# Kernel optimization log

Measured on AMD Instinct MI355X. Metric: run time of the kernel, lower is better.

Reference implementation:

```python
import jax, jax.numpy as jnp
import numpy as np
import math

B, S = 1, 2048
HID = 4096
NH = 32            # total query heads
NKV = 8            # total kv heads
D = HID // NH      # 128 head_dim
WIN = 1024         # sliding window (layer_idx=1 is odd and < num_layers//2)
LAYER = 1
THETA = 10000.0
LAMBDA_INIT = 0.8 - 0.6 * math.exp(-0.3 * LAYER)
SCALE = D ** -0.5
EPS = 1e-5
OP = NH * D + 2 * NKV * D  # Wqkv output size


def setup_inputs() -> dict:
    key = jax.random.key(0)
    ks = jax.random.split(key, 9)
    std = 0.02
    return {
        "hidden_states": jax.random.normal(ks[0], (B * S, HID), jnp.float32),
        "positions": jnp.tile(jnp.arange(S, dtype=jnp.int32), B),
        "Wqkv_w": jax.random.normal(ks[1], (OP, HID), jnp.float32) * std,
        "Wqkv_b": jnp.zeros((OP,), jnp.float32),
        "out_w": jax.random.normal(ks[2], (HID, NH * D), jnp.float32) * std,
        "out_b": jnp.zeros((HID,), jnp.float32),
        "lambda_q1": jax.random.normal(ks[3], (D,), jnp.float32) * 0.1,
        "lambda_k1": jax.random.normal(ks[4], (D,), jnp.float32) * 0.1,
        "lambda_q2": jax.random.normal(ks[5], (D,), jnp.float32) * 0.1,
        "lambda_k2": jax.random.normal(ks[6], (D,), jnp.float32) * 0.1,
        "subln_w": jnp.ones((2 * D,), jnp.float32),
    }


def _rope(x, pos):
    # neox-style rotary; x: [N, H, D], pos: [N]
    half = D // 2
    inv_freq = 1.0 / (THETA ** (jnp.arange(half, dtype=jnp.float32) / half))
    ang = pos.astype(jnp.float32)[:, None] * inv_freq[None, :]      # [N, half]
    cos = jnp.cos(ang)[:, None, :]
    sin = jnp.sin(ang)[:, None, :]
    x1, x2 = x[..., :half], x[..., half:]
    return jnp.concatenate([x1 * cos - x2 * sin, x2 * cos + x1 * sin], axis=-1)


def _probs(q, k, mask):
    # q: [B,S,Hq,D], k: [B,S,Hkv,D] -> softmax probs [B,Hq,S,S] with GQA repeat
    g = q.shape[2] // k.shape[2]
    k = jnp.repeat(k, g, axis=2)
    scores = jnp.einsum('bqhd,bkhd->bhqk', q, k) * SCALE
    scores = jnp.where(mask, scores, -1e30)
    return jax.nn.softmax(scores, axis=-1)


def _pv(p, v, g):
    # p: [B,Hq,S,S], v: [B,S,Hkv,D]
    v = jnp.repeat(v, g, axis=2)
    return jnp.einsum('bhqk,bkhd->bqhd', p, v)


def reference(hidden_states, positions, Wqkv_w, Wqkv_b, out_w, out_b,
              lambda_q1, lambda_k1, lambda_q2, lambda_k2, subln_w):
    qkv = hidden_states @ Wqkv_w.T + Wqkv_b                 # [N, OP]
    q, k, v = jnp.split(qkv, [NH * D, NH * D + NKV * D], axis=-1)
    q = q.reshape(-1, NH, D)
    k = k.reshape(-1, NKV, D)
    v = v.reshape(-1, NKV, D)
    q = _rope(q, positions)
    k = _rope(k, positions)

    q = q.reshape(B, S, NH, D)
    k = k.reshape(B, S, NKV, D)
    v = v.reshape(B, S, NKV, D)
    # split_heads: '(H two) D' -> even heads = group1, odd heads = group2
    q1, q2 = q[:, :, 0::2], q[:, :, 1::2]
    k1, k2 = k[:, :, 0::2], k[:, :, 1::2]
    v1, v2 = v[:, :, 0::2], v[:, :, 1::2]

    i = jnp.arange(S)[:, None]
    j = jnp.arange(S)[None, :]
    mask = (j <= i) & ((i - j) < WIN)                        # causal + sliding window

    g = (NH // 2) // (NKV // 2)
    p1 = _probs(q1, k1, mask)
    p2 = _probs(q2, k2, mask)
    a11 = _pv(p1, v1, g)
    a12 = _pv(p1, v2, g)
    a21 = _pv(p2, v1, g)
    a22 = _pv(p2, v2, g)

    attn1 = jnp.concatenate([a11, a12], axis=-1)             # [B,S,NH/2,2D]
    attn2 = jnp.concatenate([a21, a22], axis=-1)

    lam = (jnp.exp(jnp.sum(lambda_q1 * lambda_k1))
           - jnp.exp(jnp.sum(lambda_q2 * lambda_k2)) + LAMBDA_INIT)
    attn = attn1 - lam * attn2

    # subln: RMSNorm over last dim (2*head_dim)
    var = jnp.mean(attn * attn, axis=-1, keepdims=True)
    attn = attn * jax.lax.rsqrt(var + EPS) * subln_w
    attn = attn * (1.0 - LAMBDA_INIT)

    attn = attn.reshape(B * S, NH * D)
    return attn @ out_w.T + out_b
```

## Files before the change

### kernel.cpp

```cpp
#include <hip/hip_runtime.h>

typedef unsigned short u16;
typedef __attribute__((ext_vector_type(8))) short bf16x8;
typedef __attribute__((ext_vector_type(4))) float f32x4;
typedef __attribute__((ext_vector_type(4))) unsigned short us4;
typedef __attribute__((ext_vector_type(8))) unsigned short us8;

#define S_LEN 2048
#define QKV_P 6144
#define WIN_SZ 1024
#define SCALE_F 0.08838834764831845f
#define LAMBDA_INIT_F 0.35550906759096925f
#define ONE_MINUS_LI_F 0.6444909324090308f

__device__ __forceinline__ u16 f2bf(float f) {
    union { float f; unsigned int u; } v; v.f = f;
    unsigned int u = v.u;
    return (u16)((u + 0x7fffu + ((u >> 16) & 1u)) >> 16);
}
__device__ __forceinline__ float bf2f(u16 u) {
    union { unsigned int u; float f; } v; v.u = ((unsigned int)u) << 16; return v.f;
}
__device__ __forceinline__ void gload16(const void* g, void* l) {
    __builtin_amdgcn_global_load_lds(
        (const __attribute__((address_space(1))) unsigned int*)g,
        (__attribute__((address_space(3))) unsigned int*)l, 16, 0, 0);
}

__global__ __launch_bounds__(256)
void conv_f32_bf16(const float* __restrict__ src, u16* __restrict__ dst, int n4) {
    for (int i = blockIdx.x * 256 + threadIdx.x; i < n4; i += gridDim.x * 256) {
        float4 v = ((const float4*)src)[i];
        us4 h;
        h.x = f2bf(v.x); h.y = f2bf(v.y); h.z = f2bf(v.z); h.w = f2bf(v.w);
        ((us4*)dst)[i] = h;
    }
}

template<int NR>
__device__ __forceinline__ void stage_half(const u16* __restrict__ src, int K,
                                           int gRowBase, int kcol0,
                                           u16* slot, int tid, int wid) {
#pragma unroll
    for (int g = 0; g < 2; ++g) {
        if (g * 128 + wid * 16 < NR) {
            int row = g * 128 + (tid >> 2);
            int cc = (tid & 3) ^ ((row >> 1) & 3);
            gload16(src + (size_t)(gRowBase + row) * K + kcol0 + cc * 8,
                    slot + g * 4096 + wid * 512);
        }
    }
}

__device__ __forceinline__ bf16x8 ldfrag(const u16* slot, int row, int l4) {
    int pc = l4 ^ ((row >> 1) & 3);
    return *(const bf16x8*)(slot + row * 32 + pc * 8);
}

template<int NF>
__device__ __forceinline__ void gemm_wait(int wid) {
    if constexpr (NF == 3) {
        if (wid < 4) asm volatile("s_waitcnt vmcnt(4)" ::: "memory");
        else         asm volatile("s_waitcnt vmcnt(3)" ::: "memory");
    } else if constexpr (NF == 2) {
        asm volatile("s_waitcnt vmcnt(3)" ::: "memory");
    } else {
        asm volatile("s_waitcnt vmcnt(4)" ::: "memory");
    }
}

template<int NF, int OUT_BF16>
__global__ __launch_bounds__(512)
__attribute__((amdgpu_waves_per_eu(2, 2)))
void gemm8p(const u16* __restrict__ A, const u16* __restrict__ W,
            const float* __restrict__ bias, void* __restrict__ Cv,
            int M, int N, int K, int nbx) {
    constexpr int BN = NF * 64;
    constexpr int BSLOT = NF * 2048;
    __shared__ u16 lds[32768 + 4 * BSLOT];

    const int tid = threadIdx.x;
    const int wid = tid >> 6, lane = tid & 63;
    const int wr = wid >> 2, wc = wid & 3;
    const int l15 = lane & 15, l4 = lane >> 4;

    const int nwg = gridDim.x;
    const int q8 = nwg >> 3;
    const int swz = (blockIdx.x & 7) * q8 + (blockIdx.x >> 3);
    const int bx = swz % nbx, by = swz / nbx;
    const int rowBase = by * 256;
    const int colBase = bx * BN;

    const int NT = K >> 6;

    u16* const baseA = lds;
    u16* const baseB = lds + 32768;

    f32x4 acc[8][NF] = {};

    stage_half<256>(A, K, rowBase, 0,  baseA + 0 * 8192, tid, wid);
    stage_half<BN> (W, K, colBase, 0,  baseB + 0 * BSLOT, tid, wid);
    stage_half<256>(A, K, rowBase, 32, baseA + 1 * 8192, tid, wid);
    stage_half<BN> (W, K, colBase, 32, baseB + 1 * BSLOT, tid, wid);
    stage_half<256>(A, K, rowBase, 64, baseA + 2 * 8192, tid, wid);
    stage_half<BN> (W, K, colBase, 64, baseB + 2 * BSLOT, tid, wid);
    gemm_wait<NF>(wid);
    __builtin_amdgcn_s_barrier();

    for (int t = 0; t < NT; ++t) {
        const int b = t & 1;
        const int bn = b ^ 1;
        u16* const A0 = baseA + (b * 2 + 0) * 8192;
        u16* const A1 = baseA + (b * 2 + 1) * 8192;
        u16* const B0 = baseB + (b * 2 + 0) * BSLOT;
        u16* const B1 = baseB + (b * 2 + 1) * BSLOT;

        bf16x8 af[4], bfv[NF];

#pragma unroll
        for (int m = 0; m < 4; ++m) af[m] = ldfrag(A0, wr * 128 + m * 16 + l15, l4);
#pragma unroll
        for (int n = 0; n < NF; ++n) bfv[n] = ldfrag(B0, wc * (NF * 16) + n * 16 + l15, l4);
        if (t + 1 < NT)
            stage_half<256>(A, K, rowBase, (t + 1) * 64 + 32, baseA + (bn * 2 + 1) * 8192, tid, wid);
        __builtin_amdgcn_s_barrier();
        __builtin_amdgcn_s_setprio(1);
#pragma unroll
        for (int m = 0; m < 4; ++m)
#pragma unroll
            for (int n = 0; n < NF; ++n)
                acc[m][n] = __builtin_amdgcn_mfma_f32_16x16x32_bf16(af[m], bfv[n], acc[m][n], 0, 0, 0);
        __builtin_amdgcn_s_setprio(0);
        __builtin_amdgcn_s_barrier();

#pragma unroll
        for (int m = 0; m < 4; ++m) af[m] = ldfrag(A0, wr * 128 + (m + 4) * 16 + l15, l4);
        if (t + 1 < NT)
            stage_half<BN>(W, K, colBase, (t + 1) * 64 + 32, baseB + (bn * 2 + 1) * BSLOT, tid, wid);
        __builtin_amdgcn_s_barrier();
        __builtin_amdgcn_s_setprio(1);
#pragma unroll
        for (int m = 0; m < 4; ++m)
#pragma unroll
            for (int n = 0; n < NF; ++n)
                acc[m + 4][n] = __builtin_amdgcn_mfma_f32_16x16x32_bf16(af[m], bfv[n], acc[m + 4][n], 0, 0, 0);
        __builtin_amdgcn_s_setprio(0);
        __builtin_amdgcn_s_barrier();

#pragma unroll
        for (int m = 0; m < 4; ++m) af[m] = ldfrag(A1, wr * 128 + m * 16 + l15, l4);
#pragma unroll
        for (int n = 0; n < NF; ++n) bfv[n] = ldfrag(B1, wc * (NF * 16) + n * 16 + l15, l4);
        if (t + 2 < NT)
            stage_half<256>(A, K, rowBase, (t + 2) * 64, baseA + (b * 2 + 0) * 8192, tid, wid);
        __builtin_amdgcn_s_barrier();
        __builtin_amdgcn_s_setprio(1);
#pragma unroll
        for (int m = 0; m < 4; ++m)
#pragma unroll
            for (int n = 0; n < NF; ++n)
                acc[m][n] = __builtin_amdgcn_mfma_f32_16x16x32_bf16(af[m], bfv[n], acc[m][n], 0, 0, 0);
        __builtin_amdgcn_s_setprio(0);
        __builtin_amdgcn_s_barrier();

#pragma unroll
        for (int m = 0; m < 4; ++m) af[m] = ldfrag(A1, wr * 128 + (m + 4) * 16 + l15, l4);
        if (t + 2 < NT)
            stage_half<BN>(W, K, colBase, (t + 2) * 64, baseB + (b * 2 + 0) * BSLOT, tid, wid);
        __builtin_amdgcn_s_barrier();
        __builtin_amdgcn_s_setprio(1);
#pragma unroll
        for (int m = 0; m < 4; ++m)
#pragma unroll
            for (int n = 0; n < NF; ++n)
                acc[m + 4][n] = __builtin_amdgcn_mfma_f32_16x16x32_bf16(af[m], bfv[n], acc[m + 4][n], 0, 0, 0);
        __builtin_amdgcn_s_setprio(0);
        if (t + 2 < NT) gemm_wait<NF>(wid);
        else            asm volatile("s_waitcnt vmcnt(0)" ::: "memory");
        __builtin_amdgcn_s_barrier();
    }

#pragma unroll
    for (int n = 0; n < NF; ++n) {
        int col = colBase + wc * (NF * 16) + n * 16 + l15;
        float bs = bias[col];
#pragma unroll
        for (int m = 0; m < 8; ++m)
#pragma unroll
            for (int rr = 0; rr < 4; ++rr) {
                int rowi = rowBase + wr * 128 + m * 16 + l4 * 4 + rr;
                float v = acc[m][n][rr] + bs;
                if (OUT_BF16) ((u16*)Cv)[(size_t)rowi * N + col] = f2bf(v);
                else          ((float*)Cv)[(size_t)rowi * N + col] = v;
            }
    }
}

__global__ __launch_bounds__(256)
void rope_bf16(u16* __restrict__ qkv, const int* __restrict__ positions) {
    const int row = blockIdx.x;
    const float pos = (float)positions[row];
    for (int idx = threadIdx.x; idx < 640; idx += 256) {
        int head = idx >> 4;
        int g = idx & 15;
        int base = (head < 32) ? head * 128 : 4096 + (head - 32) * 128;
        u16* p = qkv + (size_t)row * QKV_P + base + g * 4;
        us4 x1 = *(us4*)p;
        us4 x2 = *(us4*)(p + 64);
#pragma unroll
        for (int j = 0; j < 4; ++j) {
            float inv_freq = __expf(-(float)(g * 4 + j) * (9.210340371976184f / 64.0f));
            float ang = pos * inv_freq;
            float s, c;
            sincosf(ang, &s, &c);
            float a = bf2f(x1[j]), b = bf2f(x2[j]);
            x1[j] = f2bf(a * c - b * s);
            x2[j] = f2bf(b * c + a * s);
        }
        *(us4*)p = x1;
        *(us4*)(p + 64) = x2;
    }
}

__global__ __launch_bounds__(256)
void vtrans(const u16* __restrict__ qkv, u16* __restrict__ vt) {
    __shared__ u16 T[128 * 72];
    const int s0 = blockIdx.x * 64;
    const int a = blockIdx.y;
    const u16* src = qkv + 5120 + a * 128;
#pragma unroll
    for (int it = 0; it < 4; ++it) {
        int idx = it * 256 + threadIdx.x;
        int s = idx >> 4;
        int c8 = idx & 15;
        us8 v = *(const us8*)(src + (size_t)(s0 + s) * QKV_P + c8 * 8);
        int sc = s >> 3, su = s & 7;
#pragma unroll
        for (int j = 0; j < 8; ++j) {
            int d = c8 * 8 + j;
            T[d * 72 + ((sc ^ ((d >> 3) & 7)) * 8 + su)] = v[j];
        }
    }
    __syncthreads();
#pragma unroll
    for (int it = 0; it < 4; ++it) {
        int idx = it * 256 + threadIdx.x;
        int d = idx >> 3, sc = idx & 7;
        us8 v = *(const us8*)&T[d * 72 + ((sc ^ ((d >> 3) & 7)) * 8)];
        *(us8*)(vt + (size_t)a * 262144 + (size_t)d * 2048 + s0 + sc * 8) = v;
    }
}

__global__ __launch_bounds__(512)
__attribute__((amdgpu_waves_per_eu(2, 2)))
void attn_bf16(const u16* __restrict__ qkv, const u16* __restrict__ vtg,
               u16* __restrict__ attnb,
               const float* __restrict__ lq1, const float* __restrict__ lk1,
               const float* __restrict__ lq2, const float* __restrict__ lk2,
               const float* __restrict__ subln) {
    __shared__ u16 Kb[2][2][64 * 128];
    __shared__ u16 Vb[2][2][128 * 64];
    __shared__ u16 Pw[8][16 * 64];

    const int tid = threadIdx.x;
    const int w = tid >> 6, lane = tid & 63;
    const int l15 = lane & 15, l4 = lane >> 4;

    const int qb = blockIdx.x & 15;
    const int h  = blockIdx.x >> 4;
    const int q0 = qb * 128;
    const int h1 = 2 * h, h2 = 2 * h + 1;
    const int a1 = 2 * (h >> 2), a2 = a1 + 1;

    bf16x8 q1f[4], q2f[4];
    {
        int qrow = q0 + w * 16 + l15;
        const u16* qp1 = qkv + (size_t)qrow * QKV_P + h1 * 128;
        const u16* qp2 = qkv + (size_t)qrow * QKV_P + h2 * 128;
#pragma unroll
        for (int kk = 0; kk < 4; ++kk) {
            q1f[kk] = *(const bf16x8*)(qp1 + kk * 32 + l4 * 8);
            q2f[kk] = *(const bf16x8*)(qp2 + kk * 32 + l4 * 8);
        }
    }

    f32x4 a11[8] = {}, a12[8] = {}, a21[8] = {}, a22[8] = {};
    float m1[4], l1[4], m2[4], l2[4];
#pragma unroll
    for (int r = 0; r < 4; ++r) { m1[r] = -1e30f; l1[r] = 0.f; m2[r] = -1e30f; l2[r] = 0.f; }

    const int kr4 = lane >> 4;
    const int kc  = lane & 15;
    const int vd8 = lane >> 3;
    const int vc  = lane & 7;

    const int tbeg = (qb >= 8) ? ((q0 - (WIN_SZ - 1)) >> 6) : 0;
    const int tend = (q0 + 127) >> 6;

#define STAGE_TILE(T, NB)                                                      \
    {                                                                          \
        const int kv0s = (T) * 64;                                             \
        _Pragma("unroll")                                                      \
        for (int s = 0; s < 2; ++s) {                                          \
            int ch = w * 2 + s;                                                \
            int krow = ch * 4 + kr4;                                           \
            int kcs = (kc ^ (krow & 7)) * 8;                                   \
            const u16* kbase = qkv + (size_t)(kv0s + krow) * QKV_P + 4096;     \
            gload16(kbase + a1 * 128 + kcs, &Kb[NB][0][ch * 512]);             \
            gload16(kbase + a2 * 128 + kcs, &Kb[NB][1][ch * 512]);             \
            int vdrow = ch * 8 + vd8;                                          \
            int vcs = (vc ^ (vdrow & 7)) * 8;                                  \
            const u16* vbase = vtg + (size_t)vdrow * 2048 + kv0s + vcs;        \
            gload16(vbase + (size_t)a1 * 262144, &Vb[NB][0][ch * 512]);        \
            gload16(vbase + (size_t)a2 * 262144, &Vb[NB][1][ch * 512]);        \
        }                                                                      \
    }

    STAGE_TILE(tbeg, 0);
    asm volatile("s_waitcnt vmcnt(0)" ::: "memory");
    __builtin_amdgcn_s_barrier();
    asm volatile("" ::: "memory");

    int cb = 0;
    for (int t = tbeg; t <= tend; ++t) {
        const int kv0 = t * 64;

        if (t < tend) STAGE_TILE(t + 1, cb ^ 1);

        f32x4 sc1[4], sc2[4];
        __builtin_amdgcn_s_setprio(1);
#pragma unroll
        for (int c = 0; c < 4; ++c) {
            f32x4 s1 = {0.f, 0.f, 0.f, 0.f};
            f32x4 s2 = {0.f, 0.f, 0.f, 0.f};
#pragma unroll
            for (int kk = 0; kk < 4; ++kk) {
                int off = (c * 16 + l15) * 128 + (((kk * 4 + l4) ^ (l15 & 7)) * 8);
                bf16x8 kf1 = *(const bf16x8*)&Kb[cb][0][off];
                bf16x8 kf2 = *(const bf16x8*)&Kb[cb][1][off];
                s1 = __builtin_amdgcn_mfma_f32_16x16x32_bf16(q1f[kk], kf1, s1, 0, 0, 0);
                s2 = __builtin_amdgcn_mfma_f32_16x16x32_bf16(q2f[kk], kf2, s2, 0, 0, 0);
            }
            sc1[c] = s1; sc2[c] = s2;
        }
        __builtin_amdgcn_s_setprio(0);

        const bool dz = (t >= tend - 1);
        const bool wz = (qb >= 8) && (t <= tbeg + 1);
        if (dz) {
#pragma unroll
            for (int c = 0; c < 4; ++c) {
                int j = kv0 + c * 16 + l15;
#pragma unroll
                for (int r = 0; r < 4; ++r) {
                    int i = q0 + w * 16 + l4 * 4 + r;
                    if (j > i) { sc1[c][r] = -1e30f; sc2[c][r] = -1e30f; }
                }
            }
        } else if (wz) {
#pragma unroll
            for (int c = 0; c < 4; ++c) {
                int j = kv0 + c * 16 + l15;
#pragma unroll
                for (int r = 0; r < 4; ++r) {
                    int i = q0 + w * 16 + l4 * 4 + r;
                    if (i - j >= WIN_SZ) { sc1[c][r] = -1e30f; sc2[c][r] = -1e30f; }
                }
            }
        }

        float rmax1[4], rmax2[4];
#pragma unroll
        for (int r = 0; r < 4; ++r) {
            rmax1[r] = fmaxf(fmaxf(sc1[0][r], sc1[1][r]), fmaxf(sc1[2][r], sc1[3][r]));
            rmax2[r] = fmaxf(fmaxf(sc2[0][r], sc2[1][r]), fmaxf(sc2[2][r], sc2[3][r]));
        }
#pragma unroll
        for (int msk = 1; msk < 16; msk <<= 1)
#pragma unroll
            for (int r = 0; r < 4; ++r) {
                rmax1[r] = fmaxf(rmax1[r], __shfl_xor(rmax1[r], msk));
                rmax2[r] = fmaxf(rmax2[r], __shfl_xor(rmax2[r], msk));
            }
        bool need = false;
#pragma unroll
        for (int r = 0; r < 4; ++r)
            need = need || (rmax1[r] > m1[r] + 32.0f) || (rmax2[r] > m2[r] + 32.0f);
        if (__any(need)) {
            float f1[4], f2[4];
#pragma unroll
            for (int r = 0; r < 4; ++r) {
                float nm1 = fmaxf(m1[r], rmax1[r]);
                float nm2 = fmaxf(m2[r], rmax2[r]);
                f1[r] = __expf((m1[r] - nm1) * SCALE_F);
                f2[r] = __expf((m2[r] - nm2) * SCALE_F);
                m1[r] = nm1; m2[r] = nm2;
                l1[r] *= f1[r]; l2[r] *= f2[r];
            }
#pragma unroll
            for (int f = 0; f < 8; ++f)
#pragma unroll
                for (int r = 0; r < 4; ++r) {
                    a11[f][r] *= f1[r]; a12[f][r] *= f1[r];
                    a21[f][r] *= f2[r]; a22[f][r] *= f2[r];
                }
        }

        float rs1[4] = {0.f, 0.f, 0.f, 0.f}, rs2[4] = {0.f, 0.f, 0.f, 0.f};
#pragma unroll
        for (int c = 0; c < 4; ++c) {
            int col = c * 16 + l15;
#pragma unroll
            for (int r = 0; r < 4; ++r) {
                int prow = l4 * 4 + r;
                float p1 = __expf((sc1[c][r] - m1[r]) * SCALE_F);
                float p2 = __expf((sc2[c][r] - m2[r]) * SCALE_F);
                if (wz) {
                    if (m1[r] < -1e29f) p1 = 0.f;
                    if (m2[r] < -1e29f) p2 = 0.f;
                }
                rs1[r] += p1; rs2[r] += p2;
                sc2[c][r] = p2;
                int pco = ((col >> 3) ^ (prow & 7)) * 8 + (col & 7);
                Pw[w][prow * 64 + pco] = f2bf(p1);
            }
        }
#pragma unroll
        for (int msk = 1; msk < 16; msk <<= 1)
#pragma unroll
            for (int r = 0; r < 4; ++r) {
                rs1[r] += __shfl_xor(rs1[r], msk);
                rs2[r] += __shfl_xor(rs2[r], msk);
            }
#pragma unroll
        for (int r = 0; r < 4; ++r) { l1[r] += rs1[r]; l2[r] += rs2[r]; }

        __builtin_amdgcn_s_setprio(1);
#pragma unroll
        for (int kk = 0; kk < 2; ++kk) {
            int pch = ((kk * 4 + l4) ^ (l15 & 7)) * 8;
            bf16x8 pa = *(const bf16x8*)&Pw[w][l15 * 64 + pch];
#pragma unroll
            for (int f = 0; f < 8; ++f) {
                int off = (f * 16 + l15) * 64 + (((kk * 4 + l4) ^ (l15 & 7)) * 8);
                bf16x8 vb1 = *(const bf16x8*)&Vb[cb][0][off];
                bf16x8 vb2 = *(const bf16x8*)&Vb[cb][1][off];
                a11[f] = __builtin_amdgcn_mfma_f32_16x16x32_bf16(pa, vb1, a11[f], 0, 0, 0);
                a12[f] = __builtin_amdgcn_mfma_f32_16x16x32_bf16(pa, vb2, a12[f], 0, 0, 0);
            }
        }
        __builtin_amdgcn_s_setprio(0);

#pragma unroll
        for (int c = 0; c < 4; ++c) {
            int col = c * 16 + l15;
#pragma unroll
            for (int r = 0; r < 4; ++r) {
                int prow = l4 * 4 + r;
                int pco = ((col >> 3) ^ (prow & 7)) * 8 + (col & 7);
                Pw[w][prow * 64 + pco] = f2bf(sc2[c][r]);
            }
        }
        __builtin_amdgcn_s_setprio(1);
#pragma unroll
        for (int kk = 0; kk < 2; ++kk) {
            int pch = ((kk * 4 + l4) ^ (l15 & 7)) * 8;
            bf16x8 pa = *(const bf16x8*)&Pw[w][l15 * 64 + pch];
#pragma unroll
            for (int f = 0; f < 8; ++f) {
                int off = (f * 16 + l15) * 64 + (((kk * 4 + l4) ^ (l15 & 7)) * 8);
                bf16x8 vb1 = *(const bf16x8*)&Vb[cb][0][off];
                bf16x8 vb2 = *(const bf16x8*)&Vb[cb][1][off];
                a21[f] = __builtin_amdgcn_mfma_f32_16x16x32_bf16(pa, vb1, a21[f], 0, 0, 0);
                a22[f] = __builtin_amdgcn_mfma_f32_16x16x32_bf16(pa, vb2, a22[f], 0, 0, 0);
            }
        }
        __builtin_amdgcn_s_setprio(0);

        asm volatile("s_waitcnt vmcnt(0)" ::: "memory");
        __builtin_amdgcn_s_barrier();
        asm volatile("" ::: "memory");
        cb ^= 1;
    }

    float s1v = lq1[lane] * lk1[lane] + lq1[lane + 64] * lk1[lane + 64];
    float s2v = lq2[lane] * lk2[lane] + lq2[lane + 64] * lk2[lane + 64];
#pragma unroll
    for (int msk = 1; msk < 64; msk <<= 1) {
        s1v += __shfl_xor(s1v, msk);
        s2v += __shfl_xor(s2v, msk);
    }
    const float lam = __expf(s1v) - __expf(s2v) + LAMBDA_INIT_F;

    float sw0[8], sw1[8];
#pragma unroll
    for (int f = 0; f < 8; ++f) {
        sw0[f] = subln[f * 16 + l15];
        sw1[f] = subln[128 + f * 16 + l15];
    }

#pragma unroll
    for (int r = 0; r < 4; ++r) {
        float inv1 = 1.0f / l1[r];
        float inv2 = 1.0f / l2[r];
        float o0[8], o1[8];
        float ssq = 0.f;
#pragma unroll
        for (int f = 0; f < 8; ++f) {
            o0[f] = a11[f][r] * inv1 - lam * (a21[f][r] * inv2);
            o1[f] = a12[f][r] * inv1 - lam * (a22[f][r] * inv2);
            ssq += o0[f] * o0[f] + o1[f] * o1[f];
        }
#pragma unroll
        for (int msk = 1; msk < 16; msk <<= 1) ssq += __shfl_xor(ssq, msk);
        float scale = rsqrtf(ssq * (1.0f / 256.0f) + 1e-5f) * ONE_MINUS_LI_F;
        int row = q0 + w * 16 + l4 * 4 + r;
        u16* op = attnb + (size_t)row * 4096 + h * 256;
#pragma unroll
        for (int f = 0; f < 8; ++f) {
            op[f * 16 + l15]       = f2bf(o0[f] * scale * sw0[f]);
            op[128 + f * 16 + l15] = f2bf(o1[f] * scale * sw1[f]);
        }
    }
}

extern "C" void kernel_launch(void* const* d_in, const int* in_sizes, int n_in,
                              void* d_out, int out_size, void* d_ws, size_t ws_size,
                              hipStream_t stream) {
    const float* hidden    = (const float*)d_in[0];
    const int*   positions = (const int*)d_in[1];
    const float* Wqkv_w    = (const float*)d_in[2];
    const float* Wqkv_b    = (const float*)d_in[3];
    const float* out_w     = (const float*)d_in[4];
    const float* out_b     = (const float*)d_in[5];
    const float* lq1       = (const float*)d_in[6];
    const float* lk1       = (const float*)d_in[7];
    const float* lq2       = (const float*)d_in[8];
    const float* lk2       = (const float*)d_in[9];
    const float* subln     = (const float*)d_in[10];
    float* out = (float*)d_out;

    u16* ws0   = (u16*)d_ws;
    u16* hb    = ws0;
    u16* wqb   = ws0 + 8388608;
    u16* qkvb  = ws0 + 33554432;
    u16* attnb = ws0;
    u16* owb   = ws0 + 8388608;
    u16* vt    = ws0 + 25165824;

    conv_f32_bf16<<<2048, 256, 0, stream>>>(hidden, hb, 2048 * 4096 / 4);
    conv_f32_bf16<<<2048, 256, 0, stream>>>(Wqkv_w, wqb, 6144 * 4096 / 4);

    gemm8p<3, 1><<<256, 512, 0, stream>>>(hb, wqb, Wqkv_b, qkvb, 2048, 6144, 4096, 32);

    rope_bf16<<<S_LEN, 256, 0, stream>>>(qkvb, positions);
    vtrans<<<dim3(32, 8), 256, 0, stream>>>(qkvb, vt);

    conv_f32_bf16<<<2048, 256, 0, stream>>>(out_w, owb, 4096 * 4096 / 4);

    attn_bf16<<<256, 512, 0, stream>>>(qkvb, vt, attnb, lq1, lk1, lq2, lk2, subln);

    gemm8p<2, 0><<<256, 512, 0, stream>>>(attnb, owb, out_b, out, 2048, 4096, 4096, 32);
}
```

Before: 407.6 us.

## Split attention heads across wave groups and halve query tile per block

The attention kernel now uses 64-row query tiles and 512 blocks. Within a block, waves 0-3 handle the first differential head and waves 4-7 the second, where before every wave handled both heads. Each wave keeps one softmax state and two PV accumulators, which lowers register pressure, and the two halves are combined through shared memory at the end. Heavy blocks are issued first to balance the load. In exchange, each K/V tile is loaded by more blocks, and the final combine adds a shared-memory pass and a block-wide barrier.

```diff
diff --git a/kernel.cpp b/kernel.cpp
--- a/kernel.cpp
+++ b/kernel.cpp
@@ -258,61 +258,61 @@
                const float* __restrict__ lq1, const float* __restrict__ lk1,
                const float* __restrict__ lq2, const float* __restrict__ lk2,
                const float* __restrict__ subln) {
-    __shared__ u16 Kb[2][2][64 * 128];
-    __shared__ u16 Vb[2][2][128 * 64];
-    __shared__ u16 Pw[8][16 * 64];
+    __shared__ u16 smem[73728];
+#define KBUF(b, st) (smem + ((b) * 2 + (st)) * 8192)
+#define VBUF(b, st) (smem + 32768 + ((b) * 2 + (st)) * 8192)
 
     const int tid = threadIdx.x;
     const int w = tid >> 6, lane = tid & 63;
+    const int g = w & 3, sid = w >> 2;
     const int l15 = lane & 15, l4 = lane >> 4;
-
-    const int qb = blockIdx.x & 15;
-    const int h  = blockIdx.x >> 4;
-    const int q0 = qb * 128;
-    const int h1 = 2 * h, h2 = 2 * h + 1;
+    u16* const Pw = smem + 65536 + w * 1024;
+
+    int qb, h;
+    {
+        int i = blockIdx.x;
+        if (i < 256) { qb = 16 + (i & 15); h = i >> 4; }
+        else         { int j = i - 256; qb = j & 15; h = j >> 4; }
+    }
+    const int q0 = qb * 64;
     const int a1 = 2 * (h >> 2), a2 = a1 + 1;
 
-    bf16x8 q1f[4], q2f[4];
+    bf16x8 qf[4];
     {
-        int qrow = q0 + w * 16 + l15;
-        const u16* qp1 = qkv + (size_t)qrow * QKV_P + h1 * 128;
-        const u16* qp2 = qkv + (size_t)qrow * QKV_P + h2 * 128;
-#pragma unroll
-        for (int kk = 0; kk < 4; ++kk) {
-            q1f[kk] = *(const bf16x8*)(qp1 + kk * 32 + l4 * 8);
-            q2f[kk] = *(const bf16x8*)(qp2 + kk * 32 + l4 * 8);
-        }
-    }
-
-    f32x4 a11[8] = {}, a12[8] = {}, a21[8] = {}, a22[8] = {};
-    float m1[4], l1[4], m2[4], l2[4];
-#pragma unroll
-    for (int r = 0; r < 4; ++r) { m1[r] = -1e30f; l1[r] = 0.f; m2[r] = -1e30f; l2[r] = 0.f; }
-
-    const int kr4 = lane >> 4;
-    const int kc  = lane & 15;
-    const int vd8 = lane >> 3;
-    const int vc  = lane & 7;
-
-    const int tbeg = (qb >= 8) ? ((q0 - (WIN_SZ - 1)) >> 6) : 0;
-    const int tend = (q0 + 127) >> 6;
+        int qrow = q0 + g * 16 + l15;
+        const u16* qp = qkv + (size_t)qrow * QKV_P + (2 * h + sid) * 128;
+#pragma unroll
+        for (int kk = 0; kk < 4; ++kk)
+            qf[kk] = *(const bf16x8*)(qp + kk * 32 + l4 * 8);
+    }
+
+    f32x4 aV1[8] = {}, aV2[8] = {};
+    float m[4], l[4];
+#pragma unroll
+    for (int r = 0; r < 4; ++r) { m[r] = -1e30f; l[r] = 0.f; }
+
+    const int kr4 = lane >> 4, kc = lane & 15;
+    const int vd8 = lane >> 3, vc = lane & 7;
+
+    const int tbeg = (qb >= 16) ? (qb - 16) : 0;
+    const int tend = qb;
 
 #define STAGE_TILE(T, NB)                                                      \
     {                                                                          \
         const int kv0s = (T) * 64;                                             \
         _Pragma("unroll")                                                      \
-        for (int s = 0; s < 2; ++s) {                                          \
-            int ch = w * 2 + s;                                                \
+        for (int s2 = 0; s2 < 2; ++s2) {                                       \
+            int ch = w * 2 + s2;                                               \
             int krow = ch * 4 + kr4;                                           \
             int kcs = (kc ^ (krow & 7)) * 8;                                   \
             const u16* kbase = qkv + (size_t)(kv0s + krow) * QKV_P + 4096;     \
-            gload16(kbase + a1 * 128 + kcs, &Kb[NB][0][ch * 512]);             \
-            gload16(kbase + a2 * 128 + kcs, &Kb[NB][1][ch * 512]);             \
+            gload16(kbase + a1 * 128 + kcs, KBUF(NB, 0) + ch * 512);           \
+            gload16(kbase + a2 * 128 + kcs, KBUF(NB, 1) + ch * 512);           \
             int vdrow = ch * 8 + vd8;                                          \
             int vcs = (vc ^ (vdrow & 7)) * 8;                                  \
             const u16* vbase = vtg + (size_t)vdrow * 2048 + kv0s + vcs;        \
-            gload16(vbase + (size_t)a1 * 262144, &Vb[NB][0][ch * 512]);        \
-            gload16(vbase + (size_t)a2 * 262144, &Vb[NB][1][ch * 512]);        \
+            gload16(vbase + (size_t)a1 * 262144, VBUF(NB, 0) + ch * 512);      \
+            gload16(vbase + (size_t)a2 * 262144, VBUF(NB, 1) + ch * 512);      \
         }                                                                      \
     }
 
@@ -327,34 +327,31 @@
 
         if (t < tend) STAGE_TILE(t + 1, cb ^ 1);
 
-        f32x4 sc1[4], sc2[4];
+        f32x4 sc[4];
+        const u16* Kc = KBUF(cb, sid);
         __builtin_amdgcn_s_setprio(1);
 #pragma unroll
         for (int c = 0; c < 4; ++c) {
             f32x4 s1 = {0.f, 0.f, 0.f, 0.f};
-            f32x4 s2 = {0.f, 0.f, 0.f, 0.f};
 #pragma unroll
             for (int kk = 0; kk < 4; ++kk) {
                 int off = (c * 16 + l15) * 128 + (((kk * 4 + l4) ^ (l15 & 7)) * 8);
-                bf16x8 kf1 = *(const bf16x8*)&Kb[cb][0][off];
-                bf16x8 kf2 = *(const bf16x8*)&Kb[cb][1][off];
-                s1 = __builtin_amdgcn_mfma_f32_16x16x32_bf16(q1f[kk], kf1, s1, 0, 0, 0);
-                s2 = __builtin_amdgcn_mfma_f32_16x16x32_bf16(q2f[kk], kf2, s2, 0, 0, 0);
-            }
-            sc1[c] = s1; sc2[c] = s2;
+                s1 = __builtin_amdgcn_mfma_f32_16x16x32_bf16(qf[kk], *(const bf16x8*)&Kc[off], s1, 0, 0, 0);
+            }
+            sc[c] = s1;
         }
         __builtin_amdgcn_s_setprio(0);
 
-        const bool dz = (t >= tend - 1);
-        const bool wz = (qb >= 8) && (t <= tbeg + 1);
+        const bool dz = (t == tend);
+        const bool wz = (qb >= 16) && (t <= tbeg + 1);
         if (dz) {
 #pragma unroll
             for (int c = 0; c < 4; ++c) {
                 int j = kv0 + c * 16 + l15;
 #pragma unroll
                 for (int r = 0; r < 4; ++r) {
-                    int i = q0 + w * 16 + l4 * 4 + r;
-                    if (j > i) { sc1[c][r] = -1e30f; sc2[c][r] = -1e30f; }
+                    int i = q0 + g * 16 + l4 * 4 + r;
+                    if (j > i) sc[c][r] = -1e30f;
                 }
             }
         } else if (wz) {
@@ -363,116 +360,77 @@
                 int j = kv0 + c * 16 + l15;
 #pragma unroll
                 for (int r = 0; r < 4; ++r) {
-                    int i = q0 + w * 16 + l4 * 4 + r;
-                    if (i - j >= WIN_SZ) { sc1[c][r] = -1e30f; sc2[c][r] = -1e30f; }
+                    int i = q0 + g * 16 + l4 * 4 + r;
+                    if (i - j >= WIN_SZ) sc[c][r] = -1e30f;
                 }
             }
         }
 
-        float rmax1[4], rmax2[4];
-#pragma unroll
-        for (int r = 0; r < 4; ++r) {
-            rmax1[r] = fmaxf(fmaxf(sc1[0][r], sc1[1][r]), fmaxf(sc1[2][r], sc1[3][r]));
-            rmax2[r] = fmaxf(fmaxf(sc2[0][r], sc2[1][r]), fmaxf(sc2[2][r], sc2[3][r]));
-        }
+        float rmax[4];
+#pragma unroll
+        for (int r = 0; r < 4; ++r)
+            rmax[r] = fmaxf(fmaxf(sc[0][r], sc[1][r]), fmaxf(sc[2][r], sc[3][r]));
 #pragma unroll
         for (int msk = 1; msk < 16; msk <<= 1)
 #pragma unroll
+            for (int r = 0; r < 4; ++r)
+                rmax[r] = fmaxf(rmax[r], __shfl_xor(rmax[r], msk));
+        bool need = false;
+#pragma unroll
+        for (int r = 0; r < 4; ++r)
+            need = need || (rmax[r] > m[r] + 32.0f);
+        if (__any(need)) {
+            float fr[4];
+#pragma unroll
             for (int r = 0; r < 4; ++r) {
-                rmax1[r] = fmaxf(rmax1[r], __shfl_xor(rmax1[r], msk));
-                rmax2[r] = fmaxf(rmax2[r], __shfl_xor(rmax2[r], msk));
-            }
-        bool need = false;
-#pragma unroll
-        for (int r = 0; r < 4; ++r)
-            need = need || (rmax1[r] > m1[r] + 32.0f) || (rmax2[r] > m2[r] + 32.0f);
-        if (__any(need)) {
-            float f1[4], f2[4];
-#pragma unroll
-            for (int r = 0; r < 4; ++r) {
-                float nm1 = fmaxf(m1[r], rmax1[r]);
-                float nm2 = fmaxf(m2[r], rmax2[r]);
-                f1[r] = __expf((m1[r] - nm1) * SCALE_F);
-                f2[r] = __expf((m2[r] - nm2) * SCALE_F);
-                m1[r] = nm1; m2[r] = nm2;
-                l1[r] *= f1[r]; l2[r] *= f2[r];
+                float nm = fmaxf(m[r], rmax[r]);
+                fr[r] = __expf((m[r] - nm) * SCALE_F);
+                m[r] = nm;
+                l[r] *= fr[r];
             }
 #pragma unroll
             for (int f = 0; f < 8; ++f)
 #pragma unroll
                 for (int r = 0; r < 4; ++r) {
-                    a11[f][r] *= f1[r]; a12[f][r] *= f1[r];
-                    a21[f][r] *= f2[r]; a22[f][r] *= f2[r];
+                    aV1[f][r] *= fr[r];
+                    aV2[f][r] *= fr[r];
                 }
         }
 
-        float rs1[4] = {0.f, 0.f, 0.f, 0.f}, rs2[4] = {0.f, 0.f, 0.f, 0.f};
+        float rs[4] = {0.f, 0.f, 0.f, 0.f};
 #pragma unroll
         for (int c = 0; c < 4; ++c) {
             int col = c * 16 + l15;
 #pragma unroll
             for (int r = 0; r < 4; ++r) {
                 int prow = l4 * 4 + r;
-                float p1 = __expf((sc1[c][r] - m1[r]) * SCALE_F);
-                float p2 = __expf((sc2[c][r] - m2[r]) * SCALE_F);
-                if (wz) {
-                    if (m1[r] < -1e29f) p1 = 0.f;
-                    if (m2[r] < -1e29f) p2 = 0.f;
-                }
-                rs1[r] += p1; rs2[r] += p2;
-                sc2[c][r] = p2;
+                float p = __expf((sc[c][r] - m[r]) * SCALE_F);
+                if (wz && (m[r] < -1e29f)) p = 0.f;
+                rs[r] += p;
                 int pco = ((col >> 3) ^ (prow & 7)) * 8 + (col & 7);
-                Pw[w][prow * 64 + pco] = f2bf(p1);
+                Pw[prow * 64 + pco] = f2bf(p);
             }
         }
 #pragma unroll
         for (int msk = 1; msk < 16; msk <<= 1)
 #pragma unroll
-            for (int r = 0; r < 4; ++r) {
-                rs1[r] += __shfl_xor(rs1[r], msk);
-                rs2[r] += __shfl_xor(rs2[r], msk);
-            }
-#pragma unroll
-        for (int r = 0; r < 4; ++r) { l1[r] += rs1[r]; l2[r] += rs2[r]; }
-
+            for (int r = 0; r < 4; ++r)
+                rs[r] += __shfl_xor(rs[r], msk);
+#pragma unroll
+        for (int r = 0; r < 4; ++r) l[r] += rs[r];
+
+        const u16* V0 = VBUF(cb, 0);
+        const u16* V1 = VBUF(cb, 1);
         __builtin_amdgcn_s_setprio(1);
 #pragma unroll
         for (int kk = 0; kk < 2; ++kk) {
             int pch = ((kk * 4 + l4) ^ (l15 & 7)) * 8;
-            bf16x8 pa = *(const bf16x8*)&Pw[w][l15 * 64 + pch];
+            bf16x8 pa = *(const bf16x8*)&Pw[l15 * 64 + pch];
 #pragma unroll
             for (int f = 0; f < 8; ++f) {
                 int off = (f * 16 + l15) * 64 + (((kk * 4 + l4) ^ (l15 & 7)) * 8);
-                bf16x8 vb1 = *(const bf16x8*)&Vb[cb][0][off];
-                bf16x8 vb2 = *(const bf16x8*)&Vb[cb][1][off];
-                a11[f] = __builtin_amdgcn_mfma_f32_16x16x32_bf16(pa, vb1, a11[f], 0, 0, 0);
-                a12[f] = __builtin_amdgcn_mfma_f32_16x16x32_bf16(pa, vb2, a12[f], 0, 0, 0);
-            }
-        }
-        __builtin_amdgcn_s_setprio(0);
-
-#pragma unroll
-        for (int c = 0; c < 4; ++c) {
-            int col = c * 16 + l15;
-#pragma unroll
-            for (int r = 0; r < 4; ++r) {
-                int prow = l4 * 4 + r;
-                int pco = ((col >> 3) ^ (prow & 7)) * 8 + (col & 7);
-                Pw[w][prow * 64 + pco] = f2bf(sc2[c][r]);
-            }
-        }
-        __builtin_amdgcn_s_setprio(1);
-#pragma unroll
-        for (int kk = 0; kk < 2; ++kk) {
-            int pch = ((kk * 4 + l4) ^ (l15 & 7)) * 8;
-            bf16x8 pa = *(const bf16x8*)&Pw[w][l15 * 64 + pch];
-#pragma unroll
-            for (int f = 0; f < 8; ++f) {
-                int off = (f * 16 + l15) * 64 + (((kk * 4 + l4) ^ (l15 & 7)) * 8);
-                bf16x8 vb1 = *(const bf16x8*)&Vb[cb][0][off];
-                bf16x8 vb2 = *(const bf16x8*)&Vb[cb][1][off];
-                a21[f] = __builtin_amdgcn_mfma_f32_16x16x32_bf16(pa, vb1, a21[f], 0, 0, 0);
-                a22[f] = __builtin_amdgcn_mfma_f32_16x16x32_bf16(pa, vb2, a22[f], 0, 0, 0);
+                aV1[f] = __builtin_amdgcn_mfma_f32_16x16x32_bf16(pa, *(const bf16x8*)&V0[off], aV1[f], 0, 0, 0);
+                aV2[f] = __builtin_amdgcn_mfma_f32_16x16x32_bf16(pa, *(const bf16x8*)&V1[off], aV2[f], 0, 0, 0);
             }
         }
         __builtin_amdgcn_s_setprio(0);
@@ -492,36 +450,53 @@
     }
     const float lam = __expf(s1v) - __expf(s2v) + LAMBDA_INIT_F;
 
-    float sw0[8], sw1[8];
-#pragma unroll
-    for (int f = 0; f < 8; ++f) {
-        sw0[f] = subln[f * 16 + l15];
-        sw1[f] = subln[128 + f * 16 + l15];
-    }
-
-#pragma unroll
-    for (int r = 0; r < 4; ++r) {
-        float inv1 = 1.0f / l1[r];
-        float inv2 = 1.0f / l2[r];
-        float o0[8], o1[8];
-        float ssq = 0.f;
+    float* const Cmb = (float*)smem;
+    if (sid == 1) {
+#pragma unroll
+        for (int r = 0; r < 4; ++r) {
+            float inv2 = lam / l[r];
+            int row = g * 16 + l4 * 4 + r;
+#pragma unroll
+            for (int f = 0; f < 8; ++f) {
+                Cmb[row * 264 + f * 16 + l15]       = aV1[f][r] * inv2;
+                Cmb[row * 264 + 128 + f * 16 + l15] = aV2[f][r] * inv2;
+            }
+        }
+    }
+    __syncthreads();
+    if (sid == 0) {
+        float sw0[8], sw1[8];
 #pragma unroll
         for (int f = 0; f < 8; ++f) {
-            o0[f] = a11[f][r] * inv1 - lam * (a21[f][r] * inv2);
-            o1[f] = a12[f][r] * inv1 - lam * (a22[f][r] * inv2);
-            ssq += o0[f] * o0[f] + o1[f] * o1[f];
-        }
-#pragma unroll
-        for (int msk = 1; msk < 16; msk <<= 1) ssq += __shfl_xor(ssq, msk);
-        float scale = rsqrtf(ssq * (1.0f / 256.0f) + 1e-5f) * ONE_MINUS_LI_F;
-        int row = q0 + w * 16 + l4 * 4 + r;
-        u16* op = attnb + (size_t)row * 4096 + h * 256;
-#pragma unroll
-        for (int f = 0; f < 8; ++f) {
-            op[f * 16 + l15]       = f2bf(o0[f] * scale * sw0[f]);
-            op[128 + f * 16 + l15] = f2bf(o1[f] * scale * sw1[f]);
-        }
-    }
+            sw0[f] = subln[f * 16 + l15];
+            sw1[f] = subln[128 + f * 16 + l15];
+        }
+#pragma unroll
+        for (int r = 0; r < 4; ++r) {
+            float inv1 = 1.0f / l[r];
+            int row = g * 16 + l4 * 4 + r;
+            float o0[8], o1[8];
+            float ssq = 0.f;
+#pragma unroll
+            for (int f = 0; f < 8; ++f) {
+                o0[f] = aV1[f][r] * inv1 - Cmb[row * 264 + f * 16 + l15];
+                o1[f] = aV2[f][r] * inv1 - Cmb[row * 264 + 128 + f * 16 + l15];
+                ssq += o0[f] * o0[f] + o1[f] * o1[f];
+            }
+#pragma unroll
+            for (int msk = 1; msk < 16; msk <<= 1) ssq += __shfl_xor(ssq, msk);
+            float scale = rsqrtf(ssq * (1.0f / 256.0f) + 1e-5f) * ONE_MINUS_LI_F;
+            u16* op = attnb + (size_t)(q0 + row) * 4096 + h * 256;
+#pragma unroll
+            for (int f = 0; f < 8; ++f) {
+                op[f * 16 + l15]       = f2bf(o0[f] * scale * sw0[f]);
+                op[128 + f * 16 + l15] = f2bf(o1[f] * scale * sw1[f]);
+            }
+        }
+    }
+#undef STAGE_TILE
+#undef KBUF
+#undef VBUF
 }
 
 extern "C" void kernel_launch(void* const* d_in, const int* in_sizes, int n_in,
@@ -558,7 +533,7 @@
 
     conv_f32_bf16<<<2048, 256, 0, stream>>>(out_w, owb, 4096 * 4096 / 4);
 
-    attn_bf16<<<256, 512, 0, stream>>>(qkvb, vt, attnb, lq1, lk1, lq2, lk2, subln);
+    attn_bf16<<<512, 512, 0, stream>>>(qkvb, vt, attnb, lq1, lk1, lq2, lk2, subln);
 
     gemm8p<2, 0><<<256, 512, 0, stream>>>(attnb, owb, out_b, out, 2048, 4096, 4096, 32);
 }
```

Result: faster. 362.9 us (-11.0%).
